# Optimization experiments

Hardware: AMD Instinct MI355X
Metric: run time of the kernel (lower is better)

## Reference

```python
import jax, jax.numpy as jnp
import numpy as np

WS = 7  # local window size
NH = 12  # num heads


def _ln(x, g, b, eps=1e-5):
    m = x.mean(-1, keepdims=True)
    v = ((x - m) ** 2).mean(-1, keepdims=True)
    return (x - m) / jnp.sqrt(v + eps) * g + b


def setup_inputs() -> dict:
    key = jax.random.key(0)
    ks = jax.random.split(key, 10)
    B, C, H, W = 8, 384, 112, 112
    r = 4
    s = lambda k, sh: jax.random.normal(k, sh, jnp.float32) * 0.02
    return {
        "x": jax.random.normal(ks[0], (B, C, H, W), jnp.float32),
        "w_qkv": s(ks[1], (3 * C, C)),
        "b_qkv": s(ks[2], (3 * C,)),
        "w_o": s(ks[3], (C, C)),
        "b_o": s(ks[4], (C,)),
        "w_c1": s(ks[5], (C // r, C)),
        "b_c1": s(ks[6], (C // r,)),
        "w_c2": s(ks[7], (C, C // r)),
        "b_c2": s(ks[8], (C,)),
        "g1": jnp.ones((C,), jnp.float32),
        "be1": jnp.zeros((C,), jnp.float32),
        "g2": jnp.ones((C,), jnp.float32),
        "be2": jnp.zeros((C,), jnp.float32),
    }


def reference(x, w_qkv, b_qkv, w_o, b_o, w_c1, b_c1, w_c2, b_c2, g1, be1, g2, be2):
    B, C, H, W = x.shape
    hd = C // NH
    Hw, Ww = H // WS, W // WS
    # window partition: [B,C,H,W] -> [B*Hw*Ww, WS*WS, C]
    win = x.reshape(B, C, Hw, WS, Ww, WS).transpose(0, 2, 4, 1, 3, 5)
    win = win.reshape(-1, C, WS * WS).transpose(0, 2, 1)
    Bn, T, _ = win.shape
    # torch MultiheadAttention: packed in_proj, scaled dot-product, out_proj
    qkv = win @ w_qkv.T + b_qkv
    q, k, v = jnp.split(qkv, 3, axis=-1)
    q = q.reshape(Bn, T, NH, hd)
    k = k.reshape(Bn, T, NH, hd)
    v = v.reshape(Bn, T, NH, hd)
    scores = jnp.einsum('bqhd,bkhd->bhqk', q, k) / jnp.sqrt(jnp.float32(hd))
    a = jax.nn.softmax(scores, axis=-1)
    o = jnp.einsum('bhqk,bkhd->bqhd', a, v).reshape(Bn, T, C)
    o = o @ w_o.T + b_o
    # window reverse: [Bn, WS*WS, C] -> [B,C,H,W]
    attn_out = o.reshape(B, Hw, Ww, WS, WS, C).transpose(0, 5, 1, 3, 2, 4).reshape(B, C, H, W)
    x = x + attn_out
    x = _ln(x.transpose(0, 2, 3, 1), g1, be1).transpose(0, 3, 1, 2)
    # 1x1 conv -> Mish -> 1x1 conv
    h = jnp.einsum('bchw,oc->bohw', x, w_c1) + b_c1[None, :, None, None]
    h = h * jnp.tanh(jax.nn.softplus(h))
    h = jnp.einsum('bchw,oc->bohw', h, w_c2) + b_c2[None, :, None, None]
    x = x + h
    x = _ln(x.transpose(0, 2, 3, 1), g2, be2).transpose(0, 3, 1, 2)
    return x
```

## Files before the change

kernel.cpp:

```cpp
#include <hip/hip_runtime.h>

typedef unsigned short u16;
typedef unsigned int u32;
typedef __bf16 bf16x8 __attribute__((ext_vector_type(8)));
typedef float f32x4 __attribute__((ext_vector_type(4)));

#define NPIX 100352
#define CDIM 384

static __device__ __forceinline__ u16 f2bf(float f) {
  union { float f; u32 u; } un; un.f = f;
  u32 u = un.u;
  return (u16)((u + 0x7fffu + ((u >> 16) & 1u)) >> 16);
}

static __device__ __forceinline__ f32x4 mfma_bf16(bf16x8 a, bf16x8 b, f32x4 c) {
  return __builtin_amdgcn_mfma_f32_16x16x32_bf16(a, b, c, 0, 0, 0);
}

static __device__ __forceinline__ void gload_lds16(const u16* g, u16* l) {
  __builtin_amdgcn_global_load_lds((const __attribute__((address_space(1))) void*)g,
                                   (__attribute__((address_space(3))) void*)l, 16, 0, 0);
}

__global__ __launch_bounds__(256) void k_pad_bf16(const float* __restrict__ src,
                                                  u16* __restrict__ dst,
                                                  int R, int Csrc, int Rp, int Cp) {
  int idx = blockIdx.x * 256 + threadIdx.x;
  if (idx >= Rp * Cp) return;
  int r = idx / Cp, c = idx - r * Cp;
  float v = (r < R && c < Csrc) ? src[r * Csrc + c] : 0.f;
  dst[idx] = f2bf(v);
}

__global__ __launch_bounds__(256) void k_gather(const float* __restrict__ x,
                                                float* __restrict__ xw_f32,
                                                u16* __restrict__ xw_bf16) {
  int bid = blockIdx.x;
  int cg = bid % 6;
  int tmp = bid / 6;
  int hh = tmp % 112;
  int b = tmp / 112;
  __shared__ float tile[64][113];
  int tid = threadIdx.x;
  const float* src = x + (((size_t)b * 384 + cg * 64) * 112 + hh) * 112;
  for (int idx = tid; idx < 64 * 112; idx += 256) {
    int c = idx / 112, w = idx - c * 112;
    tile[c][w] = src[(size_t)c * 12544 + w];
  }
  __syncthreads();
  int wh = hh / 7, i = hh - wh * 7;
  for (int idx = tid; idx < 64 * 112; idx += 256) {
    int w = idx >> 6, c = idx & 63;
    int ww = w / 7, j = w - ww * 7;
    size_t t = (((size_t)b * 16 + wh) * 16 + ww) * 49 + i * 7 + j;
    float v = tile[c][w];
    size_t o = t * 384 + cg * 64 + c;
    xw_f32[o] = v;
    xw_bf16[o] = f2bf(v);
  }
}

__global__ __launch_bounds__(256) void k_scatter(const float* __restrict__ t_in,
                                                 float* __restrict__ out) {
  int bid = blockIdx.x;
  int cg = bid % 6;
  int tmp = bid / 6;
  int hh = tmp % 112;
  int b = tmp / 112;
  __shared__ float tile[64][113];
  int tid = threadIdx.x;
  int wh = hh / 7, i = hh - wh * 7;
  for (int idx = tid; idx < 64 * 112; idx += 256) {
    int w = idx >> 6, c = idx & 63;
    int ww = w / 7, j = w - ww * 7;
    size_t t = (((size_t)b * 16 + wh) * 16 + ww) * 49 + i * 7 + j;
    tile[c][w] = t_in[t * 384 + cg * 64 + c];
  }
  __syncthreads();
  float* dst = out + (((size_t)b * 384 + cg * 64) * 112 + hh) * 112;
  for (int idx = tid; idx < 64 * 112; idx += 256) {
    int c = idx / 112, w = idx - c * 112;
    dst[(size_t)c * 12544 + w] = tile[c][w];
  }
}

template <int OUT_BF16, int MISH>
__global__ __launch_bounds__(256) void k_gemm(const u16* __restrict__ A,
                                              const u16* __restrict__ B,
                                              const float* __restrict__ bias, int bias_n,
                                              void* __restrict__ C, int K, int ldc) {
  __shared__ u16 lA[128 * 64];
  __shared__ u16 lB[128 * 64];
  int tid = threadIdx.x;
  int nbn = gridDim.x;
  int nwg = nbn * gridDim.y;
  int id = blockIdx.y * nbn + blockIdx.x;
  int q = nwg >> 3;
  int id2 = (id & 7) * q + (id >> 3);
  int n0 = (id2 % nbn) * 128;
  int m0 = (id2 / nbn) * 128;
  int wave = tid >> 6, lane = tid & 63;
  int wr = wave >> 1, wc = wave & 1;
  int lr = lane & 15, lg = lane >> 4;
  int lrow = lane >> 3, lchunk = lane & 7;
  int csw = (lchunk ^ lrow) << 3;
  int rsw = lr & 7;
  f32x4 acc[4][4] = {};
  int kt_n = K >> 6;
  for (int kt = 0; kt < kt_n; ++kt) {
    int k0 = kt << 6;
#pragma unroll
    for (int i = 0; i < 4; ++i) {
      int r0 = i * 32 + wave * 8;
      int row = r0 + lrow;
      gload_lds16(A + (size_t)(m0 + row) * K + k0 + csw, &lA[r0 << 6]);
      gload_lds16(B + (size_t)(n0 + row) * K + k0 + csw, &lB[r0 << 6]);
    }
    __syncthreads();
#pragma unroll
    for (int ks = 0; ks < 2; ++ks) {
      int coff = (((ks << 2) + lg) ^ rsw) << 3;
      bf16x8 af[4], bf[4];
#pragma unroll
      for (int f = 0; f < 4; ++f) {
        af[f] = *(const bf16x8*)(&lA[((wr * 64 + f * 16 + lr) << 6) + coff]);
        bf[f] = *(const bf16x8*)(&lB[((wc * 64 + f * 16 + lr) << 6) + coff]);
      }
#pragma unroll
      for (int fm = 0; fm < 4; ++fm)
#pragma unroll
        for (int fn = 0; fn < 4; ++fn)
          acc[fm][fn] = mfma_bf16(af[fm], bf[fn], acc[fm][fn]);
    }
    __syncthreads();
  }
#pragma unroll
  for (int fm = 0; fm < 4; ++fm)
#pragma unroll
    for (int fn = 0; fn < 4; ++fn) {
      int col = n0 + wc * 64 + fn * 16 + lr;
      float bi = (col < bias_n) ? bias[col] : 0.f;
#pragma unroll
      for (int r = 0; r < 4; ++r) {
        int row = m0 + wr * 64 + fm * 16 + lg * 4 + r;
        float v = acc[fm][fn][r] + bi;
        if (MISH) {
          float sp = (v > 20.f) ? v : log1pf(__expf(v));
          v = v * tanhf(sp);
        }
        if (OUT_BF16)
          ((u16*)C)[(size_t)row * ldc + col] = f2bf(v);
        else
          ((float*)C)[(size_t)row * ldc + col] = v;
      }
    }
}

__global__ __launch_bounds__(256) void k_attn(const u16* __restrict__ qkv,
                                              u16* __restrict__ o) {
  __shared__ u16 VT[4][32 * 64];
  __shared__ u16 P[4][64 * 64];
  int tid = threadIdx.x, wave = tid >> 6, lane = tid & 63;
  int gid = blockIdx.x * 4 + wave;
  int win = gid / 12, head = gid - win * 12;
  size_t tb = (size_t)win * 49;
  const u16* q_base = qkv + tb * 1152 + head * 32;
  const u16* k_base = q_base + 384;
  const u16* v_base = q_base + 768;
  u16* vt = VT[wave];
  u16* pp = P[wave];
  int lr = lane & 15, lg = lane >> 4, lk = lg << 3;

  {
    int tok = lane;
    if (tok < 49) {
      const u32* vr = (const u32*)(v_base + (size_t)tok * 1152);
#pragma unroll
      for (int q8 = 0; q8 < 4; ++q8) {
        uint4 a = *(const uint4*)(vr + q8 * 4);
        u32 arr[4] = {a.x, a.y, a.z, a.w};
#pragma unroll
        for (int p = 0; p < 4; ++p) {
          int d = q8 * 8 + p * 2;
          vt[d * 64 + tok] = (u16)(arr[p] & 0xffffu);
          vt[(d + 1) * 64 + tok] = (u16)(arr[p] >> 16);
        }
      }
    } else {
#pragma unroll
      for (int d = 0; d < 32; ++d) vt[d * 64 + tok] = 0;
    }
  }

  f32x4 sc[4][4] = {};
  {
    bf16x8 qf[4], kf[4];
#pragma unroll
    for (int f = 0; f < 4; ++f) {
      int tq = f * 16 + lr; if (tq > 48) tq = 48;
      qf[f] = *(const bf16x8*)(q_base + (size_t)tq * 1152 + lk);
      kf[f] = *(const bf16x8*)(k_base + (size_t)tq * 1152 + lk);
    }
#pragma unroll
    for (int fm = 0; fm < 4; ++fm)
#pragma unroll
      for (int fn = 0; fn < 4; ++fn)
        sc[fm][fn] = mfma_bf16(qf[fm], kf[fn], sc[fm][fn]);
  }

  const float scale = 0.17677669529663687f;
  float denom[4][4];
#pragma unroll
  for (int fm = 0; fm < 4; ++fm)
#pragma unroll
    for (int r = 0; r < 4; ++r) {
      float mx = -1e30f;
#pragma unroll
      for (int fn = 0; fn < 4; ++fn) {
        int col = fn * 16 + lr;
        float s = sc[fm][fn][r] * scale;
        if (col >= 49) s = -1e30f;
        sc[fm][fn][r] = s;
        mx = fmaxf(mx, s);
      }
      for (int off = 8; off; off >>= 1) mx = fmaxf(mx, __shfl_xor(mx, off));
      float sum = 0.f;
#pragma unroll
      for (int fn = 0; fn < 4; ++fn) {
        float e = __expf(sc[fm][fn][r] - mx);
        sc[fm][fn][r] = e;
        sum += e;
      }
      for (int off = 8; off; off >>= 1) sum += __shfl_xor(sum, off);
      denom[fm][r] = sum;
    }

#pragma unroll
  for (int fm = 0; fm < 4; ++fm)
#pragma unroll
    for (int fn = 0; fn < 4; ++fn) {
      int col = fn * 16 + lr;
#pragma unroll
      for (int r = 0; r < 4; ++r) {
        int row = fm * 16 + lg * 4 + r;
        pp[row * 64 + col] = f2bf(sc[fm][fn][r]);
      }
    }
  __syncthreads();

  f32x4 oa[4][2] = {};
#pragma unroll
  for (int ks = 0; ks < 2; ++ks) {
    bf16x8 pf[4], vf[2];
#pragma unroll
    for (int f = 0; f < 4; ++f)
      pf[f] = *(const bf16x8*)(&pp[(f * 16 + lr) * 64 + ks * 32 + lk]);
#pragma unroll
    for (int f = 0; f < 2; ++f)
      vf[f] = *(const bf16x8*)(&vt[(f * 16 + lr) * 64 + ks * 32 + lk]);
#pragma unroll
    for (int fm = 0; fm < 4; ++fm)
#pragma unroll
      for (int fn = 0; fn < 2; ++fn)
        oa[fm][fn] = mfma_bf16(pf[fm], vf[fn], oa[fm][fn]);
  }

#pragma unroll
  for (int fm = 0; fm < 4; ++fm)
#pragma unroll
    for (int fn = 0; fn < 2; ++fn)
#pragma unroll
      for (int r = 0; r < 4; ++r) {
        int q = fm * 16 + lg * 4 + r;
        if (q < 49) {
          float v = oa[fm][fn][r] / denom[fm][r];
          int d = fn * 16 + lr;
          o[(tb + q) * 384 + head * 32 + d] = f2bf(v);
        }
      }
}

template <int WRITE_BF16>
__global__ __launch_bounds__(256) void k_ln(const float* __restrict__ a,
                                            const float* __restrict__ bres,
                                            const float* __restrict__ g,
                                            const float* __restrict__ be,
                                            float* __restrict__ yf,
                                            u16* __restrict__ yb) {
  int wave = threadIdx.x >> 6, lane = threadIdx.x & 63;
  size_t t = (size_t)blockIdx.x * 4 + wave;
  const float* ar = a + t * 384;
  const float* br = bres + t * 384;
  float v[6];
  float s = 0.f, s2 = 0.f;
#pragma unroll
  for (int p = 0; p < 3; ++p) {
    int idx = p * 128 + lane * 2;
    float2 x1 = *(const float2*)(ar + idx);
    float2 x2 = *(const float2*)(br + idx);
    float a0 = x1.x + x2.x, a1 = x1.y + x2.y;
    v[p * 2] = a0; v[p * 2 + 1] = a1;
    s += a0 + a1; s2 += a0 * a0 + a1 * a1;
  }
  for (int off = 32; off; off >>= 1) {
    s += __shfl_xor(s, off);
    s2 += __shfl_xor(s2, off);
  }
  float mean = s * (1.f / 384.f);
  float var = s2 * (1.f / 384.f) - mean * mean;
  float rs = rsqrtf(var + 1e-5f);
  float* yr = yf + t * 384;
#pragma unroll
  for (int p = 0; p < 3; ++p) {
    int idx = p * 128 + lane * 2;
    float2 gg = *(const float2*)(g + idx);
    float2 bb = *(const float2*)(be + idx);
    float y0 = (v[p * 2] - mean) * rs * gg.x + bb.x;
    float y1 = (v[p * 2 + 1] - mean) * rs * gg.y + bb.y;
    *(float2*)(yr + idx) = make_float2(y0, y1);
    if (WRITE_BF16) {
      u32 pk = (u32)f2bf(y0) | ((u32)f2bf(y1) << 16);
      *(u32*)(yb + t * 384 + idx) = pk;
    }
  }
}

extern "C" void kernel_launch(void* const* d_in, const int* in_sizes, int n_in,
                              void* d_out, int out_size, void* d_ws, size_t ws_size,
                              hipStream_t stream) {
  const float* x     = (const float*)d_in[0];
  const float* w_qkv = (const float*)d_in[1];
  const float* b_qkv = (const float*)d_in[2];
  const float* w_o   = (const float*)d_in[3];
  const float* b_o   = (const float*)d_in[4];
  const float* w_c1  = (const float*)d_in[5];
  const float* b_c1  = (const float*)d_in[6];
  const float* w_c2  = (const float*)d_in[7];
  const float* b_c2  = (const float*)d_in[8];
  const float* g1    = (const float*)d_in[9];
  const float* be1   = (const float*)d_in[10];
  const float* g2    = (const float*)d_in[11];
  const float* be2   = (const float*)d_in[12];

  char* ws = (char*)d_ws;
  float* xw_f32 = (float*)ws;
  u16* xw_bf16 = (u16*)(ws + 154140672);
  char* reg3 = ws + 231211008;
  u16* qkv = (u16*)reg3;
  float* attn = (float*)reg3;
  u16* h1 = (u16*)reg3;
  float* hbuf = (float*)(reg3 + 25690112);
  u16* wq_b  = (u16*)(ws + 462422016);
  u16* wo_b  = (u16*)(ws + 463306752);
  u16* wc1_b = (u16*)(ws + 463601664);
  u16* wc2_b = (u16*)(ws + 463699968);
  u16* o_b = xw_bf16;
  u16* y_b = xw_bf16;

  k_pad_bf16<<<1728, 256, 0, stream>>>(w_qkv, wq_b, 1152, 384, 1152, 384);
  k_pad_bf16<<<576, 256, 0, stream>>>(w_o, wo_b, 384, 384, 384, 384);
  k_pad_bf16<<<192, 256, 0, stream>>>(w_c1, wc1_b, 96, 384, 128, 384);
  k_pad_bf16<<<192, 256, 0, stream>>>(w_c2, wc2_b, 384, 96, 384, 128);

  k_gather<<<5376, 256, 0, stream>>>(x, xw_f32, xw_bf16);

  k_gemm<1, 0><<<dim3(9, 784), 256, 0, stream>>>(xw_bf16, wq_b, b_qkv, 1152, (void*)qkv, 384, 1152);

  k_attn<<<6144, 256, 0, stream>>>(qkv, o_b);

  k_gemm<0, 0><<<dim3(3, 784), 256, 0, stream>>>(o_b, wo_b, b_o, 384, (void*)attn, 384, 384);

  k_ln<1><<<25088, 256, 0, stream>>>(xw_f32, attn, g1, be1, xw_f32, y_b);

  k_gemm<1, 1><<<dim3(1, 784), 256, 0, stream>>>(y_b, wc1_b, b_c1, 96, (void*)h1, 384, 128);

  k_gemm<0, 0><<<dim3(3, 784), 256, 0, stream>>>(h1, wc2_b, b_c2, 384, (void*)hbuf, 128, 384);

  k_ln<0><<<25088, 256, 0, stream>>>(xw_f32, hbuf, g2, be2, xw_f32, (u16*)nullptr);

  k_scatter<<<5376, 256, 0, stream>>>(xw_f32, (float*)d_out);
}
```

Before: 1.060 ms.

## Fuse output-projection and conv2 GEMMs with residual add and LayerNorm

Adds a GEMM kernel in which each block owns 64 full rows of 384 output columns, so the bias, residual add and LayerNorm can run in the epilogue through a cross-wave LDS reduction. It replaces the separate w_o and w_c2 GEMMs and both standalone LN kernels, removing the fp32 intermediate write and re-read of the attention and MLP outputs. The trade-offs are a larger LDS footprint, 512-thread blocks, and epilogue stores that are not coalesced because lanes write scattered columns. Only 1568 blocks cover the rows, and the K loop has no double buffering.

```diff
diff --git a/kernel.cpp b/kernel.cpp
--- a/kernel.cpp
+++ b/kernel.cpp
@@ -157,6 +157,116 @@
     }
 }
 
+template <int WRITE_BF16>
+__global__ __launch_bounds__(512, 4) void k_gemm_ln(const u16* __restrict__ A,
+                                                    const u16* __restrict__ B,
+                                                    const float* __restrict__ bias,
+                                                    const float* __restrict__ resid,
+                                                    const float* __restrict__ g,
+                                                    const float* __restrict__ be,
+                                                    float* __restrict__ yf,
+                                                    u16* __restrict__ yb, int K) {
+  __shared__ u16 lA[64 * 64];
+  __shared__ u16 lB[384 * 64];
+  __shared__ float redS[8][64], redS2[8][64];
+  __shared__ float redM[64], redR[64];
+  int tid = threadIdx.x;
+  int nwg = gridDim.x;
+  int id = blockIdx.x;
+  int q = nwg >> 3;
+  int id2 = (id & 7) * q + (id >> 3);
+  int m0 = id2 * 64;
+  int wave = tid >> 6, lane = tid & 63;
+  int lr = lane & 15, lg = lane >> 4;
+  int lchunk = lane & 7;
+  int rsw = lr & 7;
+  int srow = tid >> 3;
+  f32x4 acc[4][3] = {};
+  int kt_n = K >> 6;
+  for (int kt = 0; kt < kt_n; ++kt) {
+    int k0 = kt << 6;
+    gload_lds16(A + (size_t)(m0 + srow) * K + k0 + ((lchunk ^ (srow & 7)) << 3),
+                &lA[(wave * 8) << 6]);
+#pragma unroll
+    for (int i = 0; i < 6; ++i) {
+      int row = i * 64 + srow;
+      gload_lds16(B + (size_t)row * K + k0 + ((lchunk ^ (srow & 7)) << 3),
+                  &lB[(i * 64 + wave * 8) << 6]);
+    }
+    __syncthreads();
+#pragma unroll
+    for (int ks = 0; ks < 2; ++ks) {
+      int coff = (((ks << 2) + lg) ^ rsw) << 3;
+      bf16x8 af[4], bf[3];
+#pragma unroll
+      for (int f = 0; f < 4; ++f)
+        af[f] = *(const bf16x8*)(&lA[((f * 16 + lr) << 6) + coff]);
+#pragma unroll
+      for (int f = 0; f < 3; ++f)
+        bf[f] = *(const bf16x8*)(&lB[((wave * 48 + f * 16 + lr) << 6) + coff]);
+#pragma unroll
+      for (int fm = 0; fm < 4; ++fm)
+#pragma unroll
+        for (int fn = 0; fn < 3; ++fn)
+          acc[fm][fn] = mfma_bf16(af[fm], bf[fn], acc[fm][fn]);
+    }
+    __syncthreads();
+  }
+  int col0 = wave * 48 + lr;
+  float bi[3], gg[3], bb[3];
+#pragma unroll
+  for (int fn = 0; fn < 3; ++fn) {
+    bi[fn] = bias[col0 + fn * 16];
+    gg[fn] = g[col0 + fn * 16];
+    bb[fn] = be[col0 + fn * 16];
+  }
+#pragma unroll
+  for (int fm = 0; fm < 4; ++fm)
+#pragma unroll
+    for (int r = 0; r < 4; ++r) {
+      int rloc = fm * 16 + lg * 4 + r;
+      const float* rr = resid + (size_t)(m0 + rloc) * 384 + col0;
+      float s = 0.f, s2 = 0.f;
+#pragma unroll
+      for (int fn = 0; fn < 3; ++fn) {
+        float z = acc[fm][fn][r] + bi[fn] + rr[fn * 16];
+        acc[fm][fn][r] = z;
+        s += z; s2 += z * z;
+      }
+#pragma unroll
+      for (int off = 1; off < 16; off <<= 1) {
+        s += __shfl_xor(s, off);
+        s2 += __shfl_xor(s2, off);
+      }
+      if (lr == 0) { redS[wave][rloc] = s; redS2[wave][rloc] = s2; }
+    }
+  __syncthreads();
+  if (tid < 64) {
+    float S = 0.f, S2 = 0.f;
+#pragma unroll
+    for (int w = 0; w < 8; ++w) { S += redS[w][tid]; S2 += redS2[w][tid]; }
+    float mean = S * (1.f / 384.f);
+    float var = S2 * (1.f / 384.f) - mean * mean;
+    redM[tid] = mean;
+    redR[tid] = rsqrtf(var + 1e-5f);
+  }
+  __syncthreads();
+#pragma unroll
+  for (int fm = 0; fm < 4; ++fm)
+#pragma unroll
+    for (int r = 0; r < 4; ++r) {
+      int rloc = fm * 16 + lg * 4 + r;
+      float mean = redM[rloc], rs = redR[rloc];
+      size_t rowo = (size_t)(m0 + rloc) * 384 + col0;
+#pragma unroll
+      for (int fn = 0; fn < 3; ++fn) {
+        float y = (acc[fm][fn][r] - mean) * rs * gg[fn] + bb[fn];
+        yf[rowo + fn * 16] = y;
+        if (WRITE_BF16) yb[rowo + fn * 16] = f2bf(y);
+      }
+    }
+}
+
 __global__ __launch_bounds__(256) void k_attn(const u16* __restrict__ qkv,
                                               u16* __restrict__ o) {
   __shared__ u16 VT[4][32 * 64];
@@ -279,51 +389,6 @@
           o[(tb + q) * 384 + head * 32 + d] = f2bf(v);
         }
       }
-}
-
-template <int WRITE_BF16>
-__global__ __launch_bounds__(256) void k_ln(const float* __restrict__ a,
-                                            const float* __restrict__ bres,
-                                            const float* __restrict__ g,
-                                            const float* __restrict__ be,
-                                            float* __restrict__ yf,
-                                            u16* __restrict__ yb) {
-  int wave = threadIdx.x >> 6, lane = threadIdx.x & 63;
-  size_t t = (size_t)blockIdx.x * 4 + wave;
-  const float* ar = a + t * 384;
-  const float* br = bres + t * 384;
-  float v[6];
-  float s = 0.f, s2 = 0.f;
-#pragma unroll
-  for (int p = 0; p < 3; ++p) {
-    int idx = p * 128 + lane * 2;
-    float2 x1 = *(const float2*)(ar + idx);
-    float2 x2 = *(const float2*)(br + idx);
-    float a0 = x1.x + x2.x, a1 = x1.y + x2.y;
-    v[p * 2] = a0; v[p * 2 + 1] = a1;
-    s += a0 + a1; s2 += a0 * a0 + a1 * a1;
-  }
-  for (int off = 32; off; off >>= 1) {
-    s += __shfl_xor(s, off);
-    s2 += __shfl_xor(s2, off);
-  }
-  float mean = s * (1.f / 384.f);
-  float var = s2 * (1.f / 384.f) - mean * mean;
-  float rs = rsqrtf(var + 1e-5f);
-  float* yr = yf + t * 384;
-#pragma unroll
-  for (int p = 0; p < 3; ++p) {
-    int idx = p * 128 + lane * 2;
-    float2 gg = *(const float2*)(g + idx);
-    float2 bb = *(const float2*)(be + idx);
-    float y0 = (v[p * 2] - mean) * rs * gg.x + bb.x;
-    float y1 = (v[p * 2 + 1] - mean) * rs * gg.y + bb.y;
-    *(float2*)(yr + idx) = make_float2(y0, y1);
-    if (WRITE_BF16) {
-      u32 pk = (u32)f2bf(y0) | ((u32)f2bf(y1) << 16);
-      *(u32*)(yb + t * 384 + idx) = pk;
-    }
-  }
 }
 
 extern "C" void kernel_launch(void* const* d_in, const int* in_sizes, int n_in,
@@ -348,9 +413,7 @@
   u16* xw_bf16 = (u16*)(ws + 154140672);
   char* reg3 = ws + 231211008;
   u16* qkv = (u16*)reg3;
-  float* attn = (float*)reg3;
   u16* h1 = (u16*)reg3;
-  float* hbuf = (float*)(reg3 + 25690112);
   u16* wq_b  = (u16*)(ws + 462422016);
   u16* wo_b  = (u16*)(ws + 463306752);
   u16* wc1_b = (u16*)(ws + 463601664);
@@ -369,15 +432,13 @@
 
   k_attn<<<6144, 256, 0, stream>>>(qkv, o_b);
 
-  k_gemm<0, 0><<<dim3(3, 784), 256, 0, stream>>>(o_b, wo_b, b_o, 384, (void*)attn, 384, 384);
-
-  k_ln<1><<<25088, 256, 0, stream>>>(xw_f32, attn, g1, be1, xw_f32, y_b);
+  k_gemm_ln<1><<<1568, 512, 0, stream>>>(o_b, wo_b, b_o, xw_f32, g1, be1,
+                                         xw_f32, y_b, 384);
 
   k_gemm<1, 1><<<dim3(1, 784), 256, 0, stream>>>(y_b, wc1_b, b_c1, 96, (void*)h1, 384, 128);
 
-  k_gemm<0, 0><<<dim3(3, 784), 256, 0, stream>>>(h1, wc2_b, b_c2, 384, (void*)hbuf, 128, 384);
-
-  k_ln<0><<<25088, 256, 0, stream>>>(xw_f32, hbuf, g2, be2, xw_f32, (u16*)nullptr);
+  k_gemm_ln<0><<<1568, 512, 0, stream>>>(h1, wc2_b, b_c2, xw_f32, g2, be2,
+                                         xw_f32, (u16*)nullptr, 128);
 
   k_scatter<<<5376, 256, 0, stream>>>(xw_f32, (float*)d_out);
 }
```

Result: faster. 937.7 us (-11.5%).
